# Performance work log

Hardware: AMD Instinct MI355X
Metric: run time of the kernel (lower is better)

## Reference

```python
import jax, jax.numpy as jnp
import numpy as np

B, L, D = 2, 2048, 1024
H, DK, DV = 16, 64, 64
EPS = 1e-6

def setup_inputs() -> dict:
    key = jax.random.key(0)
    ks = jax.random.split(key, 10)
    s = 0.02
    q = jax.random.normal(ks[0], (B, L, D), jnp.float32)
    k = jax.random.normal(ks[1], (B, L, D), jnp.float32)
    v = jax.random.normal(ks[2], (B, L, D), jnp.float32)
    mask = jax.random.uniform(ks[3], (B, L, L)) < 0.95  # bool [B, Lq, Lk]
    w_q = jax.random.normal(ks[4], (D, H * DK), jnp.float32) * s
    w_k = jax.random.normal(ks[5], (D, H * DK), jnp.float32) * s
    w_v = jax.random.normal(ks[6], (D, H * DV), jnp.float32) * s
    w_o = jax.random.normal(ks[7], (H * DV, D), jnp.float32) * s
    ln_g = jnp.ones((D,), jnp.float32)
    ln_b = jnp.zeros((D,), jnp.float32)
    return {"q": q, "k": k, "v": v, "mask": mask,
            "w_q": w_q, "w_k": w_k, "w_v": w_v, "w_o": w_o,
            "ln_g": ln_g, "ln_b": ln_b}

def reference(q, k, v, mask, w_q, w_k, w_v, w_o, ln_g, ln_b):
    residual = q
    # QKV projections -> [B, H, L, d]
    qh = (q @ w_q).reshape(B, L, H, DK).transpose(0, 2, 1, 3)
    kh = (k @ w_k).reshape(B, L, H, DK).transpose(0, 2, 1, 3)
    vh = (v @ w_v).reshape(B, L, H, DV).transpose(0, 2, 1, 3)
    temp = jnp.asarray(DK, jnp.float32) ** 0.5
    # scores [B, H, Lq, Lk]
    scores = jnp.einsum('bhqd,bhkd->bhqk', qh / temp, kh)
    scores = jnp.where(mask[:, None, :, :], scores, -1e9)
    attn = jax.nn.softmax(scores, axis=-1)  # dropout = identity (eval)
    out = jnp.einsum('bhqk,bhkd->bhqd', attn, vh)
    out = out.transpose(0, 2, 1, 3).reshape(B, L, H * DV)
    out = out @ w_o + residual
    # LayerNorm, eps=1e-6
    mu = jnp.mean(out, axis=-1, keepdims=True)
    var = jnp.var(out, axis=-1, keepdims=True)
    out = (out - mu) * jax.lax.rsqrt(var + EPS) * ln_g + ln_b
    return out, attn
```

## Files before the change

kernel.cpp:

```cpp
#include <hip/hip_runtime.h>

#define B_ 2
#define L_ 2048
#define D_ 1024
#define H_ 16
#define DK_ 64

typedef __bf16 bf16x8 __attribute__((ext_vector_type(8)));
typedef short s16x8 __attribute__((ext_vector_type(8)));
typedef float f32x4 __attribute__((ext_vector_type(4)));

__device__ inline f32x4 mfma_bf16(s16x8 a, s16x8 b, f32x4 c) {
    return __builtin_amdgcn_mfma_f32_16x16x32_bf16(
        __builtin_bit_cast(bf16x8, a), __builtin_bit_cast(bf16x8, b), c, 0, 0, 0);
}

__device__ inline unsigned short f2bf(float f) {
    unsigned int x = __builtin_bit_cast(unsigned int, f);
    unsigned int r = (x + 0x7fffu + ((x >> 16) & 1u)) >> 16;
    return (unsigned short)r;
}

__device__ __forceinline__ s16x8 ldA8(const float* __restrict__ p) {
    f32x4 lo = *(const f32x4*)p;
    f32x4 hi = *(const f32x4*)(p + 4);
    s16x8 r;
#pragma unroll
    for (int j = 0; j < 4; ++j) { r[j] = (short)f2bf(lo[j]); r[j + 4] = (short)f2bf(hi[j]); }
    return r;
}
__device__ __forceinline__ s16x8 ldA8(const unsigned short* __restrict__ p) {
    return *(const s16x8*)p;
}

__global__ __launch_bounds__(256) void transpose_w(const float* __restrict__ src,
                                                   unsigned short* __restrict__ dst) {
    int idx = blockIdx.x * 256 + threadIdx.x;
    int k = idx >> 10, n = idx & 1023;
    dst[n * 1024 + k] = f2bf(src[idx]);
}

template <typename AT>
__device__ __forceinline__ void gemm_core(const AT* __restrict__ A,
                                          const unsigned short* __restrict__ BT,
                                          unsigned short* __restrict__ outb,
                                          float* __restrict__ outf, int mode) {
    __shared__ unsigned short As[128 * 32];
    __shared__ unsigned short Bs[128 * 32];
    int tid = threadIdx.x;
    int wave = tid >> 6, lane = tid & 63;
    int l15 = lane & 15, quad = lane >> 4;
    int wm = wave >> 1, wn = wave & 1;
    int m0 = blockIdx.x * 128;
    int n0 = blockIdx.y * 128;

    int f0 = wave * 1024 + lane * 8;
    int f1 = f0 + 512;
    int r0 = f0 >> 5, c0 = f0 & 31;
    int r1 = f1 >> 5, c1 = f1 & 31;
    int sw0 = r0 * 32 + ((((c0 >> 3) ^ ((r0 >> 1) & 3))) << 3);
    int sw1 = r1 * 32 + ((((c1 >> 3) ^ ((r1 >> 1) & 3))) << 3);

    const AT* ga0 = A + (size_t)(m0 + r0) * 1024 + c0;
    const AT* ga1 = A + (size_t)(m0 + r1) * 1024 + c1;
    const unsigned short* gb0 = BT + (size_t)(n0 + r0) * 1024 + c0;
    const unsigned short* gb1 = BT + (size_t)(n0 + r1) * 1024 + c1;

    f32x4 acc[4][4];
#pragma unroll
    for (int i = 0; i < 4; ++i)
#pragma unroll
        for (int j = 0; j < 4; ++j) acc[i][j] = (f32x4){0.f, 0.f, 0.f, 0.f};

    int rsw = ((l15 >> 1) & 3) ^ quad;

    s16x8 ra0 = ldA8(ga0), ra1 = ldA8(ga1);
    s16x8 rb0 = ldA8(gb0), rb1 = ldA8(gb1);

    for (int k0 = 0; k0 < 1024; k0 += 32) {
        __syncthreads();
        *(s16x8*)&As[sw0] = ra0;
        *(s16x8*)&As[sw1] = ra1;
        *(s16x8*)&Bs[sw0] = rb0;
        *(s16x8*)&Bs[sw1] = rb1;
        __syncthreads();

        if (k0 + 32 < 1024) {
            ra0 = ldA8(ga0 + k0 + 32);
            ra1 = ldA8(ga1 + k0 + 32);
            rb0 = ldA8(gb0 + k0 + 32);
            rb1 = ldA8(gb1 + k0 + 32);
        }

        s16x8 af[4], bfr[4];
#pragma unroll
        for (int t = 0; t < 4; ++t) {
            af[t]  = *(const s16x8*)&As[(wm * 64 + t * 16 + l15) * 32 + rsw * 8];
            bfr[t] = *(const s16x8*)&Bs[(wn * 64 + t * 16 + l15) * 32 + rsw * 8];
        }
#pragma unroll
        for (int i = 0; i < 4; ++i)
#pragma unroll
            for (int j = 0; j < 4; ++j)
                acc[i][j] = mfma_bf16(af[i], bfr[j], acc[i][j]);
    }

#pragma unroll
    for (int i = 0; i < 4; ++i) {
        int mb = m0 + wm * 64 + i * 16 + quad * 4;
#pragma unroll
        for (int j = 0; j < 4; ++j) {
            int n = n0 + wn * 64 + j * 16 + l15;
#pragma unroll
            for (int r = 0; r < 4; ++r) {
                int m = mb + r;
                float vv = acc[i][j][r];
                if (mode == 2) {
                    outf[(size_t)m * 1024 + n] = vv;
                } else {
                    int b = m >> 11, l = m & 2047, h = n >> 6, dd = n & 63;
                    if (mode == 0)
                        outb[(((size_t)(b * H_ + h) * L_) + l) * DK_ + dd] = f2bf(vv);
                    else
                        outb[(((size_t)(b * H_ + h) * DK_) + dd) * L_ + l] = f2bf(vv);
                }
            }
        }
    }
}

__global__ __launch_bounds__(256) void qkv_gemm(const float* __restrict__ q,
                                                const float* __restrict__ k,
                                                const float* __restrict__ v,
                                                const unsigned short* __restrict__ wqT,
                                                const unsigned short* __restrict__ wkT,
                                                const unsigned short* __restrict__ wvT,
                                                unsigned short* __restrict__ qh,
                                                unsigned short* __restrict__ kh,
                                                unsigned short* __restrict__ vt) {
    int z = blockIdx.z;
    const float* A           = (z == 0) ? q : (z == 1) ? k : v;
    const unsigned short* BT = (z == 0) ? wqT : (z == 1) ? wkT : wvT;
    unsigned short* o        = (z == 0) ? qh : (z == 1) ? kh : vt;
    gemm_core<float>(A, BT, o, nullptr, (z == 2) ? 1 : 0);
}

__global__ __launch_bounds__(256) void oproj_gemm(const unsigned short* __restrict__ ctx,
                                                  const unsigned short* __restrict__ woT,
                                                  float* __restrict__ pre) {
    gemm_core<unsigned short>(ctx, woT, nullptr, pre, 2);
}

__global__ __launch_bounds__(256) void attn_kernel(const unsigned short* __restrict__ qh,
                                                   const unsigned short* __restrict__ kh,
                                                   const unsigned short* __restrict__ vt,
                                                   const int* __restrict__ mask,
                                                   float* __restrict__ attn,
                                                   unsigned short* __restrict__ ctx) {
    __shared__ unsigned short pbuf[4][16][40];
    int wave = threadIdx.x >> 6, lane = threadIdx.x & 63;
    int l15 = lane & 15, quad = lane >> 4;
    int bh = blockIdx.x >> 5;
    int qt = blockIdx.x & 31;
    int b = bh >> 4;
    int q0 = qt * 64 + wave * 16;

    const unsigned short* Q = qh + (bh * L_ + q0 + l15) * DK_ + quad * 8;
    const unsigned short* K = kh + (size_t)bh * L_ * DK_;
    s16x8 a0 = *(const s16x8*)(Q);
    s16x8 a1 = *(const s16x8*)(Q + 32);

    const int* mrow[4];
#pragma unroll
    for (int r = 0; r < 4; ++r)
        mrow[r] = mask + (size_t)(b * L_ + q0 + quad * 4 + r) * L_;

    float l_l[4] = {0.f, 0.f, 0.f, 0.f};
    for (int kt = 0; kt < 128; ++kt) {
        int col = kt * 16 + l15;
        const unsigned short* Kp = K + col * DK_ + quad * 8;
        f32x4 acc = (f32x4){0.f, 0.f, 0.f, 0.f};
        acc = mfma_bf16(a0, *(const s16x8*)Kp, acc);
        acc = mfma_bf16(a1, *(const s16x8*)(Kp + 32), acc);
#pragma unroll
        for (int r = 0; r < 4; ++r) {
            float sv = mrow[r][col] ? acc[r] * 0.125f : -1e9f;
            l_l[r] += __expf(sv);
        }
    }
    float inv_l[4];
#pragma unroll
    for (int r = 0; r < 4; ++r) {
        float la = l_l[r];
        la += __shfl_xor(la, 1);
        la += __shfl_xor(la, 2);
        la += __shfl_xor(la, 4);
        la += __shfl_xor(la, 8);
        inv_l[r] = 1.0f / la;
    }

    float* arow[4];
#pragma unroll
    for (int r = 0; r < 4; ++r)
        arow[r] = attn + ((size_t)bh * L_ + q0 + quad * 4 + r) * L_;

    f32x4 oacc[4];
#pragma unroll
    for (int d = 0; d < 4; ++d) oacc[d] = (f32x4){0.f, 0.f, 0.f, 0.f};

    for (int c = 0; c < 64; ++c) {
        int n0 = c * 32;
#pragma unroll
        for (int t = 0; t < 2; ++t) {
            int col = n0 + t * 16 + l15;
            const unsigned short* Kp = K + col * DK_ + quad * 8;
            f32x4 acc = (f32x4){0.f, 0.f, 0.f, 0.f};
            acc = mfma_bf16(a0, *(const s16x8*)Kp, acc);
            acc = mfma_bf16(a1, *(const s16x8*)(Kp + 32), acc);
#pragma unroll
            for (int r = 0; r < 4; ++r) {
                float sv = mrow[r][col] ? acc[r] * 0.125f : -1e9f;
                float p = __expf(sv) * inv_l[r];
                arow[r][col] = p;
                pbuf[wave][quad * 4 + r][t * 16 + l15] = f2bf(p);
            }
        }
        s16x8 pa = *(const s16x8*)&pbuf[wave][l15][quad * 8];
#pragma unroll
        for (int d = 0; d < 4; ++d) {
            const unsigned short* Vp = vt + ((size_t)bh * DK_ + d * 16 + l15) * L_ + n0 + quad * 8;
            oacc[d] = mfma_bf16(pa, *(const s16x8*)Vp, oacc[d]);
        }
    }

    int h = bh & 15;
#pragma unroll
    for (int d = 0; d < 4; ++d) {
#pragma unroll
        for (int r = 0; r < 4; ++r) {
            int l = q0 + quad * 4 + r;
            ctx[((size_t)(b * L_ + l)) * 1024 + h * 64 + d * 16 + l15] = f2bf(oacc[d][r]);
        }
    }
}

__global__ __launch_bounds__(256) void ln_kernel(const float* __restrict__ pre,
                                                 const float* __restrict__ resid,
                                                 const float* __restrict__ g,
                                                 const float* __restrict__ beta,
                                                 float* __restrict__ out) {
    int row = blockIdx.x;
    int tid = threadIdx.x;
    const float* pr = pre + (size_t)row * 1024;
    const float* rr = resid + (size_t)row * 1024;
    float x[4], s = 0.f, sq = 0.f;
#pragma unroll
    for (int i = 0; i < 4; ++i) {
        int idx = tid + i * 256;
        x[i] = pr[idx] + rr[idx];
        s += x[i];
        sq += x[i] * x[i];
    }
    s += __shfl_xor(s, 1);  sq += __shfl_xor(sq, 1);
    s += __shfl_xor(s, 2);  sq += __shfl_xor(sq, 2);
    s += __shfl_xor(s, 4);  sq += __shfl_xor(sq, 4);
    s += __shfl_xor(s, 8);  sq += __shfl_xor(sq, 8);
    s += __shfl_xor(s, 16); sq += __shfl_xor(sq, 16);
    s += __shfl_xor(s, 32); sq += __shfl_xor(sq, 32);
    __shared__ float ssum[4], ssq[4];
    if ((tid & 63) == 0) { ssum[tid >> 6] = s; ssq[tid >> 6] = sq; }
    __syncthreads();
    s = ssum[0] + ssum[1] + ssum[2] + ssum[3];
    sq = ssq[0] + ssq[1] + ssq[2] + ssq[3];
    float mean = s * (1.0f / 1024.0f);
    float var = sq * (1.0f / 1024.0f) - mean * mean;
    float rstd = rsqrtf(var + 1e-6f);
#pragma unroll
    for (int i = 0; i < 4; ++i) {
        int idx = tid + i * 256;
        out[(size_t)row * 1024 + idx] = (x[i] - mean) * rstd * g[idx] + beta[idx];
    }
}

extern "C" void kernel_launch(void* const* d_in, const int* in_sizes, int n_in,
                              void* d_out, int out_size, void* d_ws, size_t ws_size,
                              hipStream_t stream) {
    const float* q   = (const float*)d_in[0];
    const float* k   = (const float*)d_in[1];
    const float* v   = (const float*)d_in[2];
    const int*   msk = (const int*)d_in[3];
    const float* w_q = (const float*)d_in[4];
    const float* w_k = (const float*)d_in[5];
    const float* w_v = (const float*)d_in[6];
    const float* w_o = (const float*)d_in[7];
    const float* lng = (const float*)d_in[8];
    const float* lnb = (const float*)d_in[9];

    char* ws = (char*)d_ws;
    unsigned short* wqT = (unsigned short*)(ws + 0 * (1u << 21));
    unsigned short* wkT = (unsigned short*)(ws + 1 * (1u << 21));
    unsigned short* wvT = (unsigned short*)(ws + 2 * (1u << 21));
    unsigned short* woT = (unsigned short*)(ws + 3 * (1u << 21));
    unsigned short* qh  = (unsigned short*)(ws + (8u << 20));
    unsigned short* kh  = (unsigned short*)(ws + (16u << 20));
    unsigned short* vt  = (unsigned short*)(ws + (24u << 20));
    unsigned short* ctx = (unsigned short*)(ws + (32u << 20));
    float*          pre = (float*)(ws + (8u << 20));

    float* outp  = (float*)d_out;
    float* attnf = outp + (size_t)B_ * L_ * D_;

    transpose_w<<<4096, 256, 0, stream>>>(w_q, wqT);
    transpose_w<<<4096, 256, 0, stream>>>(w_k, wkT);
    transpose_w<<<4096, 256, 0, stream>>>(w_v, wvT);
    transpose_w<<<4096, 256, 0, stream>>>(w_o, woT);

    dim3 gq(32, 8, 3);
    qkv_gemm<<<gq, 256, 0, stream>>>(q, k, v, wqT, wkT, wvT, qh, kh, vt);

    attn_kernel<<<1024, 256, 0, stream>>>(qh, kh, vt, msk, attnf, ctx);

    dim3 go(32, 8);
    oproj_gemm<<<go, 256, 0, stream>>>(ctx, woT, pre);

    ln_kernel<<<4096, 256, 0, stream>>>(pre, q, lng, lnb, outp);
}
```

Measured before the change: 1.073 ms.

## Pack attention mask into bits and stage it in LDS; tile weight transpose

A new pre-pass turns the int32 mask into per-64-query-tile bitmasks using wave ballots. The attention kernel loads its 16KB bit tile into shared memory once and tests bits, instead of reading int32 mask values from global memory in both passes for every head. This cuts the mask traffic that was repeated 32 times per query row. Separately, the weight transpose now goes through a shared-memory tile, so both its reads and its writes are coalesced. The packed mask reuses the start of the workspace where the Q weight copy lives, which is safe only because the QKV GEMM has already finished with that buffer.

Result: no change. 1.079 ms (+0.5%).

```diff
diff --git a/kernel.cpp b/kernel.cpp
--- a/kernel.cpp
+++ b/kernel.cpp
@@ -8,6 +8,7 @@
 
 typedef __bf16 bf16x8 __attribute__((ext_vector_type(8)));
 typedef short s16x8 __attribute__((ext_vector_type(8)));
+typedef unsigned short u16x4 __attribute__((ext_vector_type(4)));
 typedef float f32x4 __attribute__((ext_vector_type(4)));
 
 __device__ inline f32x4 mfma_bf16(s16x8 a, s16x8 b, f32x4 c) {
@@ -35,9 +36,47 @@
 
 __global__ __launch_bounds__(256) void transpose_w(const float* __restrict__ src,
                                                    unsigned short* __restrict__ dst) {
-    int idx = blockIdx.x * 256 + threadIdx.x;
-    int k = idx >> 10, n = idx & 1023;
-    dst[n * 1024 + k] = f2bf(src[idx]);
+    __shared__ float tile[64][65];
+    int bx = blockIdx.x & 15, by = blockIdx.x >> 4;
+    int k0 = by * 64, n0 = bx * 64;
+    int t = threadIdx.x;
+    int tr = t >> 4;
+    int tc = (t & 15) * 4;
+#pragma unroll
+    for (int i = 0; i < 4; ++i) {
+        int r = tr + i * 16;
+        f32x4 v = *(const f32x4*)&src[(size_t)(k0 + r) * 1024 + n0 + tc];
+        tile[r][tc + 0] = v[0]; tile[r][tc + 1] = v[1];
+        tile[r][tc + 2] = v[2]; tile[r][tc + 3] = v[3];
+    }
+    __syncthreads();
+#pragma unroll
+    for (int i = 0; i < 4; ++i) {
+        int n = tr + i * 16;
+        u16x4 o;
+#pragma unroll
+        for (int j = 0; j < 4; ++j) o[j] = f2bf(tile[tc + j][n]);
+        *(u16x4*)&dst[(size_t)(n0 + n) * 1024 + k0 + tc] = o;
+    }
+}
+
+__global__ __launch_bounds__(256) void mask_pack(const int* __restrict__ msk,
+                                                 unsigned int* __restrict__ bitsT) {
+    int wid = (blockIdx.x * 256 + threadIdx.x) >> 6;
+    int lane = threadIdx.x & 63;
+    int nwaves = gridDim.x * 4;
+    for (int chunk = wid; chunk < B_ * L_ * 32; chunk += nwaves) {
+        int c = chunk & 31;
+        int l = (chunk >> 5) & (L_ - 1);
+        int b = chunk >> 16;
+        int col = c * 64 + lane;
+        unsigned long long m = __ballot(msk[((size_t)b * L_ + l) * L_ + col] != 0);
+        if (lane == 0) {
+            unsigned int* p = bitsT + (((size_t)(b * 32 + (l >> 6)) * 64 + c * 2)) * 64 + (l & 63);
+            p[0]  = (unsigned int)m;
+            p[64] = (unsigned int)(m >> 32);
+        }
+    }
 }
 
 template <typename AT>
@@ -154,10 +193,11 @@
 __global__ __launch_bounds__(256) void attn_kernel(const unsigned short* __restrict__ qh,
                                                    const unsigned short* __restrict__ kh,
                                                    const unsigned short* __restrict__ vt,
-                                                   const int* __restrict__ mask,
+                                                   const unsigned int* __restrict__ mbits,
                                                    float* __restrict__ attn,
                                                    unsigned short* __restrict__ ctx) {
     __shared__ unsigned short pbuf[4][16][40];
+    __shared__ unsigned int mtile[64 * 64];
     int wave = threadIdx.x >> 6, lane = threadIdx.x & 63;
     int l15 = lane & 15, quad = lane >> 4;
     int bh = blockIdx.x >> 5;
@@ -165,27 +205,40 @@
     int b = bh >> 4;
     int q0 = qt * 64 + wave * 16;
 
+    {
+        const unsigned int* mb = mbits + (size_t)(b * 32 + qt) * 4096;
+#pragma unroll
+        for (int i = 0; i < 4; ++i) {
+            int idx = i * 1024 + threadIdx.x * 4;
+            *(uint4*)&mtile[idx] = *(const uint4*)&mb[idx];
+        }
+    }
+    __syncthreads();
+
     const unsigned short* Q = qh + (bh * L_ + q0 + l15) * DK_ + quad * 8;
     const unsigned short* K = kh + (size_t)bh * L_ * DK_;
     s16x8 a0 = *(const s16x8*)(Q);
     s16x8 a1 = *(const s16x8*)(Q + 32);
 
-    const int* mrow[4];
-#pragma unroll
-    for (int r = 0; r < 4; ++r)
-        mrow[r] = mask + (size_t)(b * L_ + q0 + quad * 4 + r) * L_;
+    int mrow_lds = wave * 16 + quad * 4;
 
     float l_l[4] = {0.f, 0.f, 0.f, 0.f};
-    for (int kt = 0; kt < 128; ++kt) {
-        int col = kt * 16 + l15;
-        const unsigned short* Kp = K + col * DK_ + quad * 8;
-        f32x4 acc = (f32x4){0.f, 0.f, 0.f, 0.f};
-        acc = mfma_bf16(a0, *(const s16x8*)Kp, acc);
-        acc = mfma_bf16(a1, *(const s16x8*)(Kp + 32), acc);
-#pragma unroll
-        for (int r = 0; r < 4; ++r) {
-            float sv = mrow[r][col] ? acc[r] * 0.125f : -1e9f;
-            l_l[r] += __expf(sv);
+    for (int c = 0; c < 64; ++c) {
+        uint4 mwv = *(const uint4*)&mtile[c * 64 + mrow_lds];
+        unsigned int mw[4] = {mwv.x, mwv.y, mwv.z, mwv.w};
+#pragma unroll
+        for (int t = 0; t < 2; ++t) {
+            int col = c * 32 + t * 16 + l15;
+            const unsigned short* Kp = K + col * DK_ + quad * 8;
+            f32x4 acc = (f32x4){0.f, 0.f, 0.f, 0.f};
+            acc = mfma_bf16(a0, *(const s16x8*)Kp, acc);
+            acc = mfma_bf16(a1, *(const s16x8*)(Kp + 32), acc);
+            int bitp = t * 16 + l15;
+#pragma unroll
+            for (int r = 0; r < 4; ++r) {
+                float sv = ((mw[r] >> bitp) & 1u) ? acc[r] * 0.125f : -1e9f;
+                l_l[r] += __expf(sv);
+            }
         }
     }
     float inv_l[4];
@@ -210,6 +263,8 @@
 
     for (int c = 0; c < 64; ++c) {
         int n0 = c * 32;
+        uint4 mwv = *(const uint4*)&mtile[c * 64 + mrow_lds];
+        unsigned int mw[4] = {mwv.x, mwv.y, mwv.z, mwv.w};
 #pragma unroll
         for (int t = 0; t < 2; ++t) {
             int col = n0 + t * 16 + l15;
@@ -217,9 +272,10 @@
             f32x4 acc = (f32x4){0.f, 0.f, 0.f, 0.f};
             acc = mfma_bf16(a0, *(const s16x8*)Kp, acc);
             acc = mfma_bf16(a1, *(const s16x8*)(Kp + 32), acc);
+            int bitp = t * 16 + l15;
 #pragma unroll
             for (int r = 0; r < 4; ++r) {
-                float sv = mrow[r][col] ? acc[r] * 0.125f : -1e9f;
+                float sv = ((mw[r] >> bitp) & 1u) ? acc[r] * 0.125f : -1e9f;
                 float p = __expf(sv) * inv_l[r];
                 arow[r][col] = p;
                 pbuf[wave][quad * 4 + r][t * 16 + l15] = f2bf(p);
@@ -306,19 +362,22 @@
     unsigned short* vt  = (unsigned short*)(ws + (24u << 20));
     unsigned short* ctx = (unsigned short*)(ws + (32u << 20));
     float*          pre = (float*)(ws + (8u << 20));
+    unsigned int*  mbits = (unsigned int*)(ws + 0);
 
     float* outp  = (float*)d_out;
     float* attnf = outp + (size_t)B_ * L_ * D_;
 
-    transpose_w<<<4096, 256, 0, stream>>>(w_q, wqT);
-    transpose_w<<<4096, 256, 0, stream>>>(w_k, wkT);
-    transpose_w<<<4096, 256, 0, stream>>>(w_v, wvT);
-    transpose_w<<<4096, 256, 0, stream>>>(w_o, woT);
+    transpose_w<<<256, 256, 0, stream>>>(w_q, wqT);
+    transpose_w<<<256, 256, 0, stream>>>(w_k, wkT);
+    transpose_w<<<256, 256, 0, stream>>>(w_v, wvT);
+    transpose_w<<<256, 256, 0, stream>>>(w_o, woT);
 
     dim3 gq(32, 8, 3);
     qkv_gemm<<<gq, 256, 0, stream>>>(q, k, v, wqT, wkT, wvT, qh, kh, vt);
 
-    attn_kernel<<<1024, 256, 0, stream>>>(qh, kh, vt, msk, attnf, ctx);
+    mask_pack<<<256, 256, 0, stream>>>(msk, mbits);
+
+    attn_kernel<<<1024, 256, 0, stream>>>(qh, kh, vt, mbits, attnf, ctx);
 
     dim3 go(32, 8);
     oproj_gemm<<<go, 256, 0, stream>>>(ctx, woT, pre);
```
